# Performance work log

Measured on AMD Instinct MI355X. Metric: run time of the kernel, lower is better.

The kernel has to match this reference:

```python
import jax, jax.numpy as jnp
import numpy as np

NU, NI, D, H, E, NQ = 200000, 100000, 64, 64, 1000000, 100000


def setup_inputs() -> dict:
    key = jax.random.key(0)
    ks = jax.random.split(key, 16)
    s = 0.05
    inp = {
        'user_emb': jax.random.normal(ks[0], (NU, D), jnp.float32) * s,
        'item_emb': jax.random.normal(ks[1], (NI, D), jnp.float32) * s,
        'W1': jax.random.normal(ks[2], (6, D, H), jnp.float32) * s,
        'b1': jnp.zeros((6, H), jnp.float32),
        'W2': jax.random.normal(ks[3], (6, H, H), jnp.float32) * s,
        'b2': jnp.zeros((6, H), jnp.float32),
        'dec_w1': jax.random.normal(ks[4], (2 * H, H), jnp.float32) * s,
        'dec_b1': jnp.zeros((H,), jnp.float32),
        'dec_w2': jax.random.normal(ks[5], (H, 4), jnp.float32) * s,
        'dec_b2': jnp.zeros((4,), jnp.float32),
    }
    for name, k in [('edge_view', ks[6]), ('edge_save', ks[7]), ('edge_buy', ks[8])]:
        src = jax.random.randint(k, (E,), 0, NU, jnp.int64 if jax.config.jax_enable_x64 else jnp.int32)
        dst = jax.random.randint(jax.random.fold_in(k, 1), (E,), 0, NI, src.dtype)
        inp[name] = jnp.stack([src, dst])  # [2, E], row0=user, row1=item
    inp['user_ids'] = jax.random.randint(ks[9], (NQ,), 0, NU, jnp.int32)
    inp['item_ids'] = jax.random.randint(ks[10], (NQ,), 0, NI, jnp.int32)
    return inp


def _gcn_conv(h_src, src, dst, n_src, n_dst, W, b):
    # GCNConv (add_self_loops=False) on a bipartite relation:
    # out[d] = sum_e 1/sqrt(deg_src[src_e]) * 1/sqrt(deg_dst[d]) * (x W)[src_e] + b
    h = h_src @ W  # [n_src, H]
    ones = jnp.ones(src.shape[0], h.dtype)
    deg_s = jax.ops.segment_sum(ones, src, num_segments=n_src)
    deg_d = jax.ops.segment_sum(ones, dst, num_segments=n_dst)
    inv_s = jnp.where(deg_s > 0, jax.lax.rsqrt(jnp.maximum(deg_s, 1.0)), 0.0)
    inv_d = jnp.where(deg_d > 0, jax.lax.rsqrt(jnp.maximum(deg_d, 1.0)), 0.0)
    norm = inv_s[src] * inv_d[dst]  # [E]
    msg = h[src] * norm[:, None]    # [E, H]  (dominant memory traffic)
    return jax.ops.segment_sum(msg, dst, num_segments=n_dst) + b


def _hetero_layer(xu, xi, edges, W, b, aggr):
    # relations 0..2: user->item (view,save,buy); 3..5: item->user (reverses)
    item_outs = jnp.stack([_gcn_conv(xu, e[0], e[1], NU, NI, W[k], b[k])
                           for k, e in enumerate(edges)])
    user_outs = jnp.stack([_gcn_conv(xi, e[1], e[0], NI, NU, W[k + 3], b[k + 3])
                           for k, e in enumerate(edges)])
    if aggr == 'max':
        return user_outs.max(0), item_outs.max(0)
    return user_outs.sum(0), item_outs.sum(0)


def reference(user_emb, item_emb, W1, b1, W2, b2, dec_w1, dec_b1, dec_w2, dec_b2,
              edge_view, edge_save, edge_buy, user_ids, item_ids):
    edges = [edge_view, edge_save, edge_buy]
    xu, xi = _hetero_layer(user_emb, item_emb, edges, W1, b1, 'max')
    xu, xi = jax.nn.relu(xu), jax.nn.relu(xi)
    xu, xi = _hetero_layer(xu, xi, edges, W2, b2, 'sum')
    edge_emb = jnp.concatenate([xu[user_ids], xi[item_ids]], axis=-1)  # [NQ, 2H]
    h = jax.nn.relu(edge_emb @ dec_w1 + dec_b1)  # dropout in eval mode = identity
    return h @ dec_w2 + dec_b2  # [NQ, 4]
```

## Files before the change

### kernel.cpp

```cpp
#include <hip/hip_runtime.h>
#include <math.h>

#define NUV 200000
#define NIV 100000
#define EV  1000000
#define NQV 100000
#define NC  (3 * NIV + 3 * NUV)

__global__ __launch_bounds__(256) void k_count(const int* __restrict__ su,
                                               const int* __restrict__ di,
                                               int* __restrict__ cnt, int k) {
    int e = blockIdx.x * 256 + threadIdx.x;
    if (e < EV) {
        atomicAdd(&cnt[k * NIV + di[e]], 1);
        atomicAdd(&cnt[3 * NIV + k * NUV + su[e]], 1);
    }
}

__global__ __launch_bounds__(256) void k_invf(const int* __restrict__ cnt,
                                              float* __restrict__ invs) {
    int i = blockIdx.x * 256 + threadIdx.x;
    if (i < NC) {
        int c = cnt[i];
        invs[i] = (c > 0) ? (1.0f / sqrtf((float)c)) : 0.0f;
    }
}

__global__ __launch_bounds__(256) void k_scan1(const int* __restrict__ cnt,
                                               int* __restrict__ S,
                                               int* __restrict__ bsum) {
    __shared__ int tmp[256];
    int idx = blockIdx.x * 256 + threadIdx.x;
    int v = (idx < NC) ? cnt[idx] : 0;
    tmp[threadIdx.x] = v;
    __syncthreads();
    for (int off = 1; off < 256; off <<= 1) {
        int t = (threadIdx.x >= off) ? tmp[threadIdx.x - off] : 0;
        __syncthreads();
        tmp[threadIdx.x] += t;
        __syncthreads();
    }
    if (idx < NC) S[idx] = tmp[threadIdx.x] - v;
    if (threadIdx.x == 255) bsum[blockIdx.x] = tmp[255];
}

__global__ __launch_bounds__(64) void k_scan2(int* __restrict__ bsum, int nb) {
    int lane = threadIdx.x;
    int carry = 0;
    for (int base = 0; base < nb; base += 64) {
        int i = base + lane;
        int v = (i < nb) ? bsum[i] : 0;
        int orig = v;
        #pragma unroll
        for (int off = 1; off < 64; off <<= 1) {
            int t = __shfl_up(v, off, 64);
            if (lane >= off) v += t;
        }
        if (i < nb) bsum[i] = carry + v - orig;
        carry += __shfl(v, 63, 64);
    }
}

__global__ __launch_bounds__(256) void k_scan3(int* __restrict__ S,
                                               const int* __restrict__ bsum) {
    int idx = blockIdx.x * 256 + threadIdx.x;
    if (idx < NC) S[idx] += bsum[blockIdx.x];
    if (idx == 0) S[NC] = 6 * EV;
}

__global__ __launch_bounds__(256) void k_fill(const int* __restrict__ su,
                                              const int* __restrict__ di,
                                              const float* __restrict__ invs,
                                              int* __restrict__ cur,
                                              float2* __restrict__ ent, int k) {
    int e = blockIdx.x * 256 + threadIdx.x;
    if (e < EV) {
        int u = su[e], i = di[e];
        float nm = invs[k * NIV + i] * invs[3 * NIV + k * NUV + u];
        int p1 = atomicAdd(&cur[k * NIV + i], 1);
        ent[p1] = make_float2(__int_as_float(u), nm);
        int p2 = atomicAdd(&cur[3 * NIV + k * NUV + u], 1);
        ent[p2] = make_float2(__int_as_float(i), nm);
    }
}

__global__ __launch_bounds__(256) void k_agg(const float* __restrict__ x_i,
                                             const float* __restrict__ x_u,
                                             const float2* __restrict__ ent,
                                             const int* __restrict__ S,
                                             const float* __restrict__ Wall,
                                             const float* __restrict__ ball,
                                             float* __restrict__ out_i,
                                             float* __restrict__ out_u,
                                             int mode) {
    __shared__ float sW[4096];
    __shared__ float sAcc[16 * 68];
    const int nb_i = NIV / 16;
    bool item_side = blockIdx.x < nb_i;
    const float* x  = item_side ? x_i : x_u;
    const float* Wb = item_side ? Wall : Wall + 3 * 4096;
    const float* bb = item_side ? ball : ball + 192;
    float* outp     = item_side ? out_i : out_u;
    int n_dst       = item_side ? NIV : NUV;
    int seg_base    = item_side ? 0 : 3 * NIV;
    int d0          = (item_side ? blockIdx.x : (blockIdx.x - nb_i)) * 16;

    int wave = threadIdx.x >> 6;
    int lane = threadIdx.x & 63;
    int eg   = lane >> 4;
    int fq   = lane & 15;
    int r2 = threadIdx.x >> 4;
    int g  = threadIdx.x & 15;

    float4 res = make_float4(0.f, 0.f, 0.f, 0.f);
    for (int k = 0; k < 3; k++) {
        __syncthreads();
        {
            const float4* wsrc = (const float4*)(Wb + (size_t)k * 4096);
            float4* wdst = (float4*)sW;
            #pragma unroll
            for (int i = 0; i < 4; i++) wdst[threadIdx.x + 256 * i] = wsrc[threadIdx.x + 256 * i];
        }
        {
            int idx = seg_base + k * n_dst + d0 + wave * 4;
            int v0 = S[idx], v1 = S[idx + 1], v2 = S[idx + 2], v3 = S[idx + 3], v4 = S[idx + 4];
            int st[4] = {v0, v1, v2, v3};
            int en[4] = {v1, v2, v3, v4};
            int maxlen = max(max(v1 - v0, v2 - v1), max(v3 - v2, v4 - v3));
            int maxit = (maxlen + 3) >> 2;
            float4 a[4];
            #pragma unroll
            for (int n = 0; n < 4; n++) a[n] = make_float4(0.f, 0.f, 0.f, 0.f);
            for (int it = 0; it < maxit; it++) {
                #pragma unroll
                for (int n = 0; n < 4; n++) {
                    int p = st[n] + (it << 2) + eg;
                    if (p < en[n]) {
                        float2 e = ent[p];
                        int s = __float_as_int(e.x);
                        float4 xv = *(const float4*)&x[(size_t)s * 64 + fq * 4];
                        a[n].x = fmaf(xv.x, e.y, a[n].x);
                        a[n].y = fmaf(xv.y, e.y, a[n].y);
                        a[n].z = fmaf(xv.z, e.y, a[n].z);
                        a[n].w = fmaf(xv.w, e.y, a[n].w);
                    }
                }
            }
            #pragma unroll
            for (int n = 0; n < 4; n++) {
                #pragma unroll
                for (int off = 16; off < 64; off <<= 1) {
                    a[n].x += __shfl_xor(a[n].x, off, 64);
                    a[n].y += __shfl_xor(a[n].y, off, 64);
                    a[n].z += __shfl_xor(a[n].z, off, 64);
                    a[n].w += __shfl_xor(a[n].w, off, 64);
                }
                if (lane < 16)
                    *(float4*)&sAcc[(wave * 4 + n) * 68 + fq * 4] = a[n];
            }
        }
        __syncthreads();
        float4 y = *(const float4*)&bb[k * 64 + g * 4];
        #pragma unroll
        for (int c = 0; c < 64; c++) {
            float a = sAcc[r2 * 68 + c];
            float4 w = *(const float4*)&sW[c * 64 + g * 4];
            y.x = fmaf(a, w.x, y.x);
            y.y = fmaf(a, w.y, y.y);
            y.z = fmaf(a, w.z, y.z);
            y.w = fmaf(a, w.w, y.w);
        }
        if (k == 0) {
            res = y;
        } else if (mode == 0) {
            res.x = fmaxf(res.x, y.x); res.y = fmaxf(res.y, y.y);
            res.z = fmaxf(res.z, y.z); res.w = fmaxf(res.w, y.w);
        } else {
            res.x += y.x; res.y += y.y; res.z += y.z; res.w += y.w;
        }
    }
    if (mode == 0) {
        res.x = fmaxf(res.x, 0.f); res.y = fmaxf(res.y, 0.f);
        res.z = fmaxf(res.z, 0.f); res.w = fmaxf(res.w, 0.f);
    }
    *(float4*)&outp[(size_t)(d0 + r2) * 64 + g * 4] = res;
}

__global__ __launch_bounds__(256) void k_decoder(const float* __restrict__ xu,
                                                 const float* __restrict__ xi,
                                                 const int* __restrict__ uids,
                                                 const int* __restrict__ iids,
                                                 const float* __restrict__ w1,
                                                 const float* __restrict__ b1,
                                                 const float* __restrict__ w2,
                                                 const float* __restrict__ b2,
                                                 float* __restrict__ out) {
    __shared__ float sW1[128 * 64];
    __shared__ float sE[16 * 132];
    __shared__ float sH[16 * 68];
    __shared__ float sW2[64 * 4];
    {
        const float4* wsrc = (const float4*)w1;
        float4* wdst = (float4*)sW1;
        #pragma unroll
        for (int i = 0; i < 8; i++) wdst[threadIdx.x + 256 * i] = wsrc[threadIdx.x + 256 * i];
        if (threadIdx.x < 64) {
            float4 v = ((const float4*)w2)[threadIdx.x];
            ((float4*)sW2)[threadIdx.x] = v;
        }
    }
    int q0 = blockIdx.x * 16;
    {
        int q = threadIdx.x >> 4;
        int p = threadIdx.x & 15;
        int uid = uids[q0 + q];
        int iid = iids[q0 + q];
        float4 vu = *(const float4*)&xu[(size_t)uid * 64 + p * 4];
        float4 vi = *(const float4*)&xi[(size_t)iid * 64 + p * 4];
        *(float4*)&sE[q * 132 + p * 4] = vu;
        *(float4*)&sE[q * 132 + 64 + p * 4] = vi;
    }
    __syncthreads();
    {
        int r = threadIdx.x >> 4;
        int g = threadIdx.x & 15;
        float4 y = *(const float4*)&b1[g * 4];
        #pragma unroll
        for (int c = 0; c < 128; c++) {
            float a = sE[r * 132 + c];
            float4 w = *(const float4*)&sW1[c * 64 + g * 4];
            y.x = fmaf(a, w.x, y.x);
            y.y = fmaf(a, w.y, y.y);
            y.z = fmaf(a, w.z, y.z);
            y.w = fmaf(a, w.w, y.w);
        }
        y.x = fmaxf(y.x, 0.f); y.y = fmaxf(y.y, 0.f);
        y.z = fmaxf(y.z, 0.f); y.w = fmaxf(y.w, 0.f);
        *(float4*)&sH[r * 68 + g * 4] = y;
    }
    __syncthreads();
    if (threadIdx.x < 64) {
        int q = threadIdx.x >> 2;
        int oc = threadIdx.x & 3;
        float acc = b2[oc];
        #pragma unroll
        for (int c = 0; c < 64; c++)
            acc = fmaf(sH[q * 68 + c], sW2[c * 4 + oc], acc);
        out[(size_t)(q0 + q) * 4 + oc] = acc;
    }
}

extern "C" void kernel_launch(void* const* d_in, const int* in_sizes, int n_in,
                              void* d_out, int out_size, void* d_ws, size_t ws_size,
                              hipStream_t stream) {
    const float* user_emb = (const float*)d_in[0];
    const float* item_emb = (const float*)d_in[1];
    const float* W1 = (const float*)d_in[2];
    const float* b1 = (const float*)d_in[3];
    const float* W2 = (const float*)d_in[4];
    const float* b2 = (const float*)d_in[5];
    const float* dw1 = (const float*)d_in[6];
    const float* db1 = (const float*)d_in[7];
    const float* dw2 = (const float*)d_in[8];
    const float* db2 = (const float*)d_in[9];
    const int* edges[3] = {(const int*)d_in[10], (const int*)d_in[11], (const int*)d_in[12]};
    const int* uids = (const int*)d_in[13];
    const int* iids = (const int*)d_in[14];
    float* out = (float*)d_out;
    (void)in_sizes; (void)n_in; (void)out_size; (void)ws_size;

    char* base = (char*)d_ws;
    size_t off = 0;
    int*    cnt  = (int*)(base + off); off += (size_t)NC * 4;
    int*    S    = (int*)(base + off); off += (size_t)(NC + 8) * 4;
    int*    cur  = (int*)(base + off); off += (size_t)(NC + 8) * 4;
    int*    bsum = (int*)(base + off); off += (size_t)4096 * 4;
    float*  invs = (float*)(base + off); off += (size_t)NC * 4;
    float2* ent  = (float2*)(base + off); off += (size_t)6 * EV * 8;
    float*  xu1  = (float*)(base + off); off += (size_t)NUV * 64 * 4;
    float*  xi1  = (float*)(base + off); off += (size_t)NIV * 64 * 4;
    float*  xu2  = (float*)(base + off); off += (size_t)NUV * 64 * 4;
    float*  xi2  = (float*)(base + off); off += (size_t)NIV * 64 * 4;

    const int EB  = (EV + 255) / 256;
    const int SB1 = (NC + 255) / 256;
    const int AGGB = NIV / 16 + NUV / 16;

    hipMemsetAsync(cnt, 0, (size_t)NC * 4, stream);
    for (int k = 0; k < 3; k++)
        k_count<<<EB, 256, 0, stream>>>(edges[k], edges[k] + EV, cnt, k);
    k_invf<<<SB1, 256, 0, stream>>>(cnt, invs);
    k_scan1<<<SB1, 256, 0, stream>>>(cnt, S, bsum);
    k_scan2<<<1, 64, 0, stream>>>(bsum, SB1);
    k_scan3<<<SB1, 256, 0, stream>>>(S, bsum);
    hipMemcpyAsync(cur, S, (size_t)NC * 4, hipMemcpyDeviceToDevice, stream);
    for (int k = 0; k < 3; k++)
        k_fill<<<EB, 256, 0, stream>>>(edges[k], edges[k] + EV, invs, cur, ent, k);

    k_agg<<<AGGB, 256, 0, stream>>>(user_emb, item_emb, ent, S, W1, b1, xi1, xu1, 0);
    k_agg<<<AGGB, 256, 0, stream>>>(xu1, xi1, ent, S, W2, b2, xi2, xu2, 1);

    k_decoder<<<NQV / 16, 256, 0, stream>>>(xu2, xi2, uids, iids,
                                            dw1, db1, dw2, db2, out);
}
```

Before: 1.682 ms.

## Gather node features in fp16, reuse count ranks for CSR fill

Converts the input embeddings and the layer-1 outputs to fp16, so the edge gather in the aggregation kernel reads half the bytes per neighbour while still accumulating in fp32. The count kernel now records each edge's atomic rank, which lets the fill kernel compute slots directly and drops the second round of atomics and the cursor copy. The aggregation kernel is templated on mode and output type, its neighbour loop is unrolled by two, and it carries an occupancy hint. The cost is fp16 rounding error, two extra conversion launches, and 24 MB of rank buffers to write and read back.

```diff
diff --git a/kernel.cpp b/kernel.cpp
--- a/kernel.cpp
+++ b/kernel.cpp
@@ -1,4 +1,5 @@
 #include <hip/hip_runtime.h>
+#include <hip/hip_fp16.h>
 #include <math.h>
 
 #define NUV 200000
@@ -7,13 +8,29 @@
 #define NQV 100000
 #define NC  (3 * NIV + 3 * NUV)
 
+struct alignas(8) H4 { __half2 a, b; };
+
+__global__ __launch_bounds__(256) void k_tohalf(const float* __restrict__ in,
+                                                __half* __restrict__ out, int n4) {
+    int i = blockIdx.x * 256 + threadIdx.x;
+    if (i < n4) {
+        float4 v = ((const float4*)in)[i];
+        H4 o;
+        o.a = __floats2half2_rn(v.x, v.y);
+        o.b = __floats2half2_rn(v.z, v.w);
+        ((H4*)out)[i] = o;
+    }
+}
+
 __global__ __launch_bounds__(256) void k_count(const int* __restrict__ su,
                                                const int* __restrict__ di,
-                                               int* __restrict__ cnt, int k) {
+                                               int* __restrict__ cnt,
+                                               int* __restrict__ rk_i,
+                                               int* __restrict__ rk_u, int k) {
     int e = blockIdx.x * 256 + threadIdx.x;
     if (e < EV) {
-        atomicAdd(&cnt[k * NIV + di[e]], 1);
-        atomicAdd(&cnt[3 * NIV + k * NUV + su[e]], 1);
+        rk_i[e] = atomicAdd(&cnt[k * NIV + di[e]], 1);
+        rk_u[e] = atomicAdd(&cnt[3 * NIV + k * NUV + su[e]], 1);
     }
 }
 
@@ -71,36 +88,38 @@
 __global__ __launch_bounds__(256) void k_fill(const int* __restrict__ su,
                                               const int* __restrict__ di,
                                               const float* __restrict__ invs,
-                                              int* __restrict__ cur,
+                                              const int* __restrict__ S,
+                                              const int* __restrict__ rk_i,
+                                              const int* __restrict__ rk_u,
                                               float2* __restrict__ ent, int k) {
     int e = blockIdx.x * 256 + threadIdx.x;
     if (e < EV) {
         int u = su[e], i = di[e];
         float nm = invs[k * NIV + i] * invs[3 * NIV + k * NUV + u];
-        int p1 = atomicAdd(&cur[k * NIV + i], 1);
+        int p1 = S[k * NIV + i] + rk_i[e];
         ent[p1] = make_float2(__int_as_float(u), nm);
-        int p2 = atomicAdd(&cur[3 * NIV + k * NUV + u], 1);
+        int p2 = S[3 * NIV + k * NUV + u] + rk_u[e];
         ent[p2] = make_float2(__int_as_float(i), nm);
     }
 }
 
-__global__ __launch_bounds__(256) void k_agg(const float* __restrict__ x_i,
-                                             const float* __restrict__ x_u,
-                                             const float2* __restrict__ ent,
-                                             const int* __restrict__ S,
-                                             const float* __restrict__ Wall,
-                                             const float* __restrict__ ball,
-                                             float* __restrict__ out_i,
-                                             float* __restrict__ out_u,
-                                             int mode) {
+template <int MODE, bool HOUT>
+__global__ __launch_bounds__(256, 4) void k_agg(const __half* __restrict__ x_i,
+                                                const __half* __restrict__ x_u,
+                                                const float2* __restrict__ ent,
+                                                const int* __restrict__ S,
+                                                const float* __restrict__ Wall,
+                                                const float* __restrict__ ball,
+                                                void* __restrict__ out_i,
+                                                void* __restrict__ out_u) {
     __shared__ float sW[4096];
     __shared__ float sAcc[16 * 68];
     const int nb_i = NIV / 16;
     bool item_side = blockIdx.x < nb_i;
-    const float* x  = item_side ? x_i : x_u;
+    const __half* x = item_side ? x_i : x_u;
     const float* Wb = item_side ? Wall : Wall + 3 * 4096;
     const float* bb = item_side ? ball : ball + 192;
-    float* outp     = item_side ? out_i : out_u;
+    void* outp      = item_side ? out_i : out_u;
     int n_dst       = item_side ? NIV : NUV;
     int seg_base    = item_side ? 0 : 3 * NIV;
     int d0          = (item_side ? blockIdx.x : (blockIdx.x - nb_i)) * 16;
@@ -115,6 +134,8 @@
     float4 res = make_float4(0.f, 0.f, 0.f, 0.f);
     for (int k = 0; k < 3; k++) {
         __syncthreads();
+        int idx = seg_base + k * n_dst + d0 + wave * 4;
+        int v0 = S[idx], v1 = S[idx + 1], v2 = S[idx + 2], v3 = S[idx + 3], v4 = S[idx + 4];
         {
             const float4* wsrc = (const float4*)(Wb + (size_t)k * 4096);
             float4* wdst = (float4*)sW;
@@ -122,8 +143,6 @@
             for (int i = 0; i < 4; i++) wdst[threadIdx.x + 256 * i] = wsrc[threadIdx.x + 256 * i];
         }
         {
-            int idx = seg_base + k * n_dst + d0 + wave * 4;
-            int v0 = S[idx], v1 = S[idx + 1], v2 = S[idx + 2], v3 = S[idx + 3], v4 = S[idx + 4];
             int st[4] = {v0, v1, v2, v3};
             int en[4] = {v1, v2, v3, v4};
             int maxlen = max(max(v1 - v0, v2 - v1), max(v3 - v2, v4 - v3));
@@ -131,18 +150,32 @@
             float4 a[4];
             #pragma unroll
             for (int n = 0; n < 4; n++) a[n] = make_float4(0.f, 0.f, 0.f, 0.f);
-            for (int it = 0; it < maxit; it++) {
+            for (int it = 0; it < maxit; it += 2) {
                 #pragma unroll
                 for (int n = 0; n < 4; n++) {
-                    int p = st[n] + (it << 2) + eg;
-                    if (p < en[n]) {
-                        float2 e = ent[p];
+                    int p0 = st[n] + (it << 2) + eg;
+                    if (p0 < en[n]) {
+                        float2 e = ent[p0];
                         int s = __float_as_int(e.x);
-                        float4 xv = *(const float4*)&x[(size_t)s * 64 + fq * 4];
-                        a[n].x = fmaf(xv.x, e.y, a[n].x);
-                        a[n].y = fmaf(xv.y, e.y, a[n].y);
-                        a[n].z = fmaf(xv.z, e.y, a[n].z);
-                        a[n].w = fmaf(xv.w, e.y, a[n].w);
+                        float2 raw = *(const float2*)(x + (size_t)s * 64 + fq * 4);
+                        float2 f0 = __half22float2(*reinterpret_cast<__half2*>(&raw.x));
+                        float2 f1 = __half22float2(*reinterpret_cast<__half2*>(&raw.y));
+                        a[n].x = fmaf(f0.x, e.y, a[n].x);
+                        a[n].y = fmaf(f0.y, e.y, a[n].y);
+                        a[n].z = fmaf(f1.x, e.y, a[n].z);
+                        a[n].w = fmaf(f1.y, e.y, a[n].w);
+                    }
+                    int p1 = p0 + 4;
+                    if (p1 < en[n]) {
+                        float2 e = ent[p1];
+                        int s = __float_as_int(e.x);
+                        float2 raw = *(const float2*)(x + (size_t)s * 64 + fq * 4);
+                        float2 f0 = __half22float2(*reinterpret_cast<__half2*>(&raw.x));
+                        float2 f1 = __half22float2(*reinterpret_cast<__half2*>(&raw.y));
+                        a[n].x = fmaf(f0.x, e.y, a[n].x);
+                        a[n].y = fmaf(f0.y, e.y, a[n].y);
+                        a[n].z = fmaf(f1.x, e.y, a[n].z);
+                        a[n].w = fmaf(f1.y, e.y, a[n].w);
                     }
                 }
             }
@@ -172,18 +205,25 @@
         }
         if (k == 0) {
             res = y;
-        } else if (mode == 0) {
+        } else if (MODE == 0) {
             res.x = fmaxf(res.x, y.x); res.y = fmaxf(res.y, y.y);
             res.z = fmaxf(res.z, y.z); res.w = fmaxf(res.w, y.w);
         } else {
             res.x += y.x; res.y += y.y; res.z += y.z; res.w += y.w;
         }
     }
-    if (mode == 0) {
+    if (MODE == 0) {
         res.x = fmaxf(res.x, 0.f); res.y = fmaxf(res.y, 0.f);
         res.z = fmaxf(res.z, 0.f); res.w = fmaxf(res.w, 0.f);
     }
-    *(float4*)&outp[(size_t)(d0 + r2) * 64 + g * 4] = res;
+    if (HOUT) {
+        H4 o;
+        o.a = __floats2half2_rn(res.x, res.y);
+        o.b = __floats2half2_rn(res.z, res.w);
+        *(H4*)((__half*)outp + (size_t)(d0 + r2) * 64 + g * 4) = o;
+    } else {
+        *(float4*)((float*)outp + (size_t)(d0 + r2) * 64 + g * 4) = res;
+    }
 }
 
 __global__ __launch_bounds__(256) void k_decoder(const float* __restrict__ xu,
@@ -271,34 +311,41 @@
 
     char* base = (char*)d_ws;
     size_t off = 0;
-    int*    cnt  = (int*)(base + off); off += (size_t)NC * 4;
-    int*    S    = (int*)(base + off); off += (size_t)(NC + 8) * 4;
-    int*    cur  = (int*)(base + off); off += (size_t)(NC + 8) * 4;
-    int*    bsum = (int*)(base + off); off += (size_t)4096 * 4;
-    float*  invs = (float*)(base + off); off += (size_t)NC * 4;
+    int*    cnt  = (int*)(base + off);    off += (size_t)NC * 4;
+    int*    S    = (int*)(base + off);    off += (size_t)(NC + 8) * 4;
+    int*    bsum = (int*)(base + off);    off += (size_t)4096 * 4;
+    float*  invs = (float*)(base + off);  off += (size_t)NC * 4;
+    int*    rki  = (int*)(base + off);    off += (size_t)3 * EV * 4;
+    int*    rku  = (int*)(base + off);    off += (size_t)3 * EV * 4;
     float2* ent  = (float2*)(base + off); off += (size_t)6 * EV * 8;
-    float*  xu1  = (float*)(base + off); off += (size_t)NUV * 64 * 4;
-    float*  xi1  = (float*)(base + off); off += (size_t)NIV * 64 * 4;
-    float*  xu2  = (float*)(base + off); off += (size_t)NUV * 64 * 4;
-    float*  xi2  = (float*)(base + off); off += (size_t)NIV * 64 * 4;
+    __half* he_u = (__half*)(base + off); off += (size_t)NUV * 64 * 2;
+    __half* he_i = (__half*)(base + off); off += (size_t)NIV * 64 * 2;
+    __half* xu1h = (__half*)(base + off); off += (size_t)NUV * 64 * 2;
+    __half* xi1h = (__half*)(base + off); off += (size_t)NIV * 64 * 2;
+    float*  xu2  = (float*)(base + off);  off += (size_t)NUV * 64 * 4;
+    float*  xi2  = (float*)(base + off);  off += (size_t)NIV * 64 * 4;
 
     const int EB  = (EV + 255) / 256;
     const int SB1 = (NC + 255) / 256;
     const int AGGB = NIV / 16 + NUV / 16;
 
+    k_tohalf<<<(NUV * 64 / 4 + 255) / 256, 256, 0, stream>>>(user_emb, he_u, NUV * 64 / 4);
+    k_tohalf<<<(NIV * 64 / 4 + 255) / 256, 256, 0, stream>>>(item_emb, he_i, NIV * 64 / 4);
+
     hipMemsetAsync(cnt, 0, (size_t)NC * 4, stream);
     for (int k = 0; k < 3; k++)
-        k_count<<<EB, 256, 0, stream>>>(edges[k], edges[k] + EV, cnt, k);
+        k_count<<<EB, 256, 0, stream>>>(edges[k], edges[k] + EV, cnt,
+                                        rki + (size_t)k * EV, rku + (size_t)k * EV, k);
     k_invf<<<SB1, 256, 0, stream>>>(cnt, invs);
     k_scan1<<<SB1, 256, 0, stream>>>(cnt, S, bsum);
     k_scan2<<<1, 64, 0, stream>>>(bsum, SB1);
     k_scan3<<<SB1, 256, 0, stream>>>(S, bsum);
-    hipMemcpyAsync(cur, S, (size_t)NC * 4, hipMemcpyDeviceToDevice, stream);
     for (int k = 0; k < 3; k++)
-        k_fill<<<EB, 256, 0, stream>>>(edges[k], edges[k] + EV, invs, cur, ent, k);
-
-    k_agg<<<AGGB, 256, 0, stream>>>(user_emb, item_emb, ent, S, W1, b1, xi1, xu1, 0);
-    k_agg<<<AGGB, 256, 0, stream>>>(xu1, xi1, ent, S, W2, b2, xi2, xu2, 1);
+        k_fill<<<EB, 256, 0, stream>>>(edges[k], edges[k] + EV, invs, S,
+                                       rki + (size_t)k * EV, rku + (size_t)k * EV, ent, k);
+
+    k_agg<0, true><<<AGGB, 256, 0, stream>>>(he_u, he_i, ent, S, W1, b1, xi1h, xu1h);
+    k_agg<1, false><<<AGGB, 256, 0, stream>>>(xu1h, xi1h, ent, S, W2, b2, xi2, xu2);
 
     k_decoder<<<NQV / 16, 256, 0, stream>>>(xu2, xi2, uids, iids,
                                             dw1, db1, dw2, db2, out);
```

New measurement: 1.471 ms. 12.5% less time.
